# Kernel optimization log

Hardware: AMD Instinct MI355X
Metric: run time of the kernel (lower is better)

The kernel has to match this reference:

```python
import jax, jax.numpy as jnp
import numpy as np

T, N, F = 8, 4096, 128
LPF, HPF, H, LP_HID, E = 128, 128, 256, 256, 131072
D = LPF + HPF


def setup_inputs() -> dict:
    key = jax.random.key(0)
    ks = jax.random.split(key, 16)
    s = lambda k, *shape: jax.random.normal(k, shape, dtype=jnp.float32) * 0.05
    feats = jax.random.normal(ks[0], (T, N, F), dtype=jnp.float32)
    # row-stochastic-ish propagation matrices
    p = jax.random.uniform(ks[1], (T, N, N), dtype=jnp.float32)
    p = p / jnp.sum(p, axis=-1, keepdims=True)
    eidx = jax.random.randint(ks[2], (2, E), 0, N, dtype=jnp.int64)
    return {
        "features": feats,
        "p_matrix": p,
        "predict_edge_index": eidx,
        "W_lpf": s(ks[3], F, LPF), "b_lpf": jnp.zeros((LPF,), jnp.float32),
        "W_hpf": s(ks[4], F, HPF), "b_hpf": jnp.zeros((HPF,), jnp.float32),
        "W_ih": s(ks[5], 4 * H, D), "W_hh": s(ks[6], 4 * H, H),
        "b_ih": jnp.zeros((4 * H,), jnp.float32), "b_hh": jnp.zeros((4 * H,), jnp.float32),
        "W1": s(ks[7], 2 * H, LP_HID), "b1": jnp.zeros((LP_HID,), jnp.float32),
        "W2": s(ks[8], LP_HID, 1), "b2": jnp.zeros((1,), jnp.float32),
    }


def reference(features, p_matrix, predict_edge_index, W_lpf, b_lpf, W_hpf, b_hpf,
              W_ih, W_hh, b_ih, b_hh, W1, b1, W2, b2):
    # --- batched low/high-pass graph filters over all T snapshots ---
    xw = jnp.einsum('tnf,fd->tnd', features, W_lpf)          # X @ W_lp
    low = jax.nn.relu(jnp.einsum('tnm,tmd->tnd', p_matrix, xw) + b_lpf)
    px = jnp.einsum('tnm,tmf->tnf', p_matrix, features)      # P @ X
    high = jax.nn.relu(jnp.einsum('tnf,fd->tnd', features - px, W_hpf) + b_hpf)
    x_seq = jnp.concatenate([low, high], axis=-1)            # [T, N, D]

    # --- LSTM over time, nodes as batch (torch gate order i,f,g,o) ---
    def step(carry, x_t):
        h, c = carry
        gates = x_t @ W_ih.T + h @ W_hh.T + (b_ih + b_hh)    # [N, 4H]
        i, f, g, o = jnp.split(gates, 4, axis=-1)
        c = jax.nn.sigmoid(f) * c + jax.nn.sigmoid(i) * jnp.tanh(g)
        h = jax.nn.sigmoid(o) * jnp.tanh(c)
        return (h, c), None

    h0 = jnp.zeros((N, H), x_seq.dtype)
    (h_fin, _), _ = jax.lax.scan(step, (h0, h0), x_seq)      # final timestep hidden

    # --- gather + concat + MLP link predictor ---
    src = h_fin[predict_edge_index[0]]
    dst = h_fin[predict_edge_index[1]]
    comb = jnp.concatenate([src, dst], axis=-1)              # [E, 2H]
    hid = jax.nn.relu(comb @ W1 + b1)
    logits = (hid @ W2 + b2).squeeze(-1)                     # [E]
    return logits
```

## Files before the change

kernel.cpp:

```cpp
#include <hip/hip_runtime.h>
#include <stdint.h>

#define T_ 8
#define N_ 4096
#define E_ 131072

typedef __attribute__((ext_vector_type(4))) float f32x4;
typedef __attribute__((ext_vector_type(8))) short s16x8;
typedef __attribute__((ext_vector_type(4))) short s16x4;

static __device__ __forceinline__ short f2bf(float f) {
    union { float f; unsigned u; } v; v.f = f;
    unsigned r = v.u + 0x7fffu + ((v.u >> 16) & 1u);
    return (short)(r >> 16);
}
static __device__ __forceinline__ float bf2f(short s) {
    union { float f; unsigned u; } v; v.u = ((unsigned)(unsigned short)s) << 16;
    return v.f;
}

static __device__ __forceinline__ void bar_nodrain() {
    asm volatile("s_waitcnt lgkmcnt(0)\n\ts_barrier" ::: "memory");
}

__global__ __launch_bounds__(256) void xw_gemm(const float* __restrict__ A,
                                               const float* __restrict__ W,
                                               float* __restrict__ C) {
    __shared__ float As[32][68];
    __shared__ float Ws[32][132];
    const int m0 = blockIdx.x * 64;
    const int tid = threadIdx.x;
    const int rg = tid & 15, cg = tid >> 4;
    float acc[4][8];
#pragma unroll
    for (int r = 0; r < 4; r++)
#pragma unroll
        for (int c = 0; c < 8; c++) acc[r][c] = 0.f;

    for (int k0 = 0; k0 < 128; k0 += 32) {
#pragma unroll
        for (int s = 0; s < 2; s++) {
            int q = tid + s * 256, row = q >> 3, k4 = q & 7;
            f32x4 v = *(const f32x4*)&A[(size_t)(m0 + row) * 128 + k0 + k4 * 4];
#pragma unroll
            for (int i = 0; i < 4; i++) As[k4 * 4 + i][row] = v[i];
        }
#pragma unroll
        for (int s = 0; s < 4; s++) {
            int q = tid + s * 256, kk = q >> 5, j4 = q & 31;
            *(f32x4*)&Ws[kk][j4 * 4] = *(const f32x4*)&W[(size_t)(k0 + kk) * 128 + j4 * 4];
        }
        __syncthreads();
#pragma unroll
        for (int kk = 0; kk < 32; kk++) {
            f32x4 a  = *(const f32x4*)&As[kk][rg * 4];
            f32x4 w0 = *(const f32x4*)&Ws[kk][cg * 8];
            f32x4 w1 = *(const f32x4*)&Ws[kk][cg * 8 + 4];
#pragma unroll
            for (int r = 0; r < 4; r++)
#pragma unroll
                for (int c = 0; c < 4; c++) {
                    acc[r][c]     += a[r] * w0[c];
                    acc[r][c + 4] += a[r] * w1[c];
                }
        }
        __syncthreads();
    }
#pragma unroll
    for (int r = 0; r < 4; r++) {
        f32x4 o0 = {acc[r][0], acc[r][1], acc[r][2], acc[r][3]};
        f32x4 o1 = {acc[r][4], acc[r][5], acc[r][6], acc[r][7]};
        size_t base = (size_t)(m0 + rg * 4 + r) * 128 + cg * 8;
        *(f32x4*)&C[base] = o0;
        *(f32x4*)&C[base + 4] = o1;
    }
}

__global__ __launch_bounds__(256) void pack_yt(const float* __restrict__ xw,
                                               const float* __restrict__ feat,
                                               short* __restrict__ yt) {
    __shared__ float tile[32][33];
    const int t = blockIdx.z, j0 = blockIdx.y * 32, n0 = blockIdx.x * 32;
    const float* src = (j0 < 128) ? (xw + (size_t)t * N_ * 128 + j0)
                                  : (feat + (size_t)t * N_ * 128 + (j0 - 128));
    const int jj = threadIdx.x & 31, i4 = threadIdx.x >> 5;
#pragma unroll
    for (int s = 0; s < 4; s++) {
        int ii = i4 * 4 + s;
        tile[ii][jj] = src[(size_t)(n0 + ii) * 128 + jj];
    }
    __syncthreads();
    const int nn = threadIdx.x & 31, j4 = threadIdx.x >> 5;
#pragma unroll
    for (int s = 0; s < 4; s++) {
        int j2 = j4 * 4 + s;
        yt[(size_t)(t * 256 + j0 + j2) * N_ + n0 + nn] = f2bf(tile[nn][j2]);
    }
}

__global__ __launch_bounds__(512) void pfy_gemm(const float* __restrict__ P,
                                                const short* __restrict__ Yt,
                                                float* __restrict__ Z) {
    __shared__ short As[2][128][72];
    __shared__ short Bs[2][256][72];
    const int t = blockIdx.y;
    const int m0 = blockIdx.x * 128;
    const int tid = threadIdx.x;
    const int lane = tid & 63, wid = tid >> 6;
    const int wm = wid >> 2, wn = wid & 3;
    const int frow = lane & 15, kq = lane >> 4;

    const float* Pt = P + (size_t)t * N_ * N_;
    const short* Bt = Yt + (size_t)t * 256 * N_;

    const int ar = tid >> 2;
    const int ak16 = (tid & 3) * 16;
    const int bj = tid >> 1;
    const int bk32 = (tid & 1) * 32;

    f32x4 acc[4][4];
    f32x4 zf = {0.f, 0.f, 0.f, 0.f};
#pragma unroll
    for (int m = 0; m < 4; m++)
#pragma unroll
        for (int n = 0; n < 4; n++) acc[m][n] = zf;

    f32x4 aA[4], aB[4]; s16x8 bA[4], bB[4];

    const float* Pr = &Pt[(size_t)(m0 + ar) * 4096 + ak16];
    const short* Br = &Bt[(size_t)bj * 4096 + bk32];

#define LOADA(KT) do { const int k0_ = (KT) * 64;                              \
        _Pragma("unroll") for (int i = 0; i < 4; i++)                          \
            aA[i] = *(const f32x4*)&Pr[k0_ + i * 4];                           \
        _Pragma("unroll") for (int i = 0; i < 4; i++)                          \
            bA[i] = *(const s16x8*)&Br[k0_ + i * 8]; } while (0)
#define LOADB(KT) do { const int k0_ = (KT) * 64;                              \
        _Pragma("unroll") for (int i = 0; i < 4; i++)                          \
            aB[i] = *(const f32x4*)&Pr[k0_ + i * 4];                           \
        _Pragma("unroll") for (int i = 0; i < 4; i++)                          \
            bB[i] = *(const s16x8*)&Br[k0_ + i * 8]; } while (0)
#define STOREA(BUF) do {                                                       \
        _Pragma("unroll") for (int i = 0; i < 4; i++) {                        \
            s16x4 c4_;                                                         \
            _Pragma("unroll") for (int j = 0; j < 4; j++) c4_[j] = f2bf(aA[i][j]); \
            *(s16x4*)&As[BUF][ar][ak16 + i * 4] = c4_; }                       \
        _Pragma("unroll") for (int i = 0; i < 4; i++)                          \
            *(s16x8*)&Bs[BUF][bj][bk32 + i * 8] = bA[i]; } while (0)
#define STOREB(BUF) do {                                                       \
        _Pragma("unroll") for (int i = 0; i < 4; i++) {                        \
            s16x4 c4_;                                                         \
            _Pragma("unroll") for (int j = 0; j < 4; j++) c4_[j] = f2bf(aB[i][j]); \
            *(s16x4*)&As[BUF][ar][ak16 + i * 4] = c4_; }                       \
        _Pragma("unroll") for (int i = 0; i < 4; i++)                          \
            *(s16x8*)&Bs[BUF][bj][bk32 + i * 8] = bB[i]; } while (0)

    auto compute_t = [&](int buf) {
#pragma unroll
        for (int ks = 0; ks < 2; ks++) {
            s16x8 af[4], bfr[4];
#pragma unroll
            for (int m = 0; m < 4; m++)
                af[m] = *(const s16x8*)&As[buf][wm * 64 + m * 16 + frow][kq * 8 + ks * 32];
#pragma unroll
            for (int n = 0; n < 4; n++)
                bfr[n] = *(const s16x8*)&Bs[buf][wn * 64 + n * 16 + frow][kq * 8 + ks * 32];
#pragma unroll
            for (int m = 0; m < 4; m++)
#pragma unroll
                for (int n = 0; n < 4; n++)
                    acc[m][n] = __builtin_amdgcn_mfma_f32_16x16x32_bf16(af[m], bfr[n], acc[m][n], 0, 0, 0);
        }
    };

    LOADA(0);
    STOREA(0);
    LOADB(1);
    LOADA(2);
    bar_nodrain();

#pragma unroll 2
    for (int kt = 0; kt < 64; kt++) {
        compute_t(kt & 1);
        if (kt < 63) {
            if ((kt & 1) == 0) {
                STOREB(1);
                if (kt + 3 < 64) LOADB(kt + 3);
            } else {
                STOREA(0);
                if (kt + 3 < 64) LOADA(kt + 3);
            }
            bar_nodrain();
        }
    }
#undef LOADA
#undef LOADB
#undef STOREA
#undef STOREB

    float* Zt = Z + (size_t)t * N_ * 256;
#pragma unroll
    for (int m = 0; m < 4; m++)
#pragma unroll
        for (int n = 0; n < 4; n++)
#pragma unroll
            for (int r = 0; r < 4; r++) {
                int row = m0 + wm * 64 + m * 16 + kq * 4 + r;
                int col = wn * 64 + n * 16 + frow;
                Zt[(size_t)row * 256 + col] = acc[m][n][r];
            }
}

__global__ __launch_bounds__(256) void hp_gemm(const float* __restrict__ feat,
                                               const float* __restrict__ Z,
                                               const float* __restrict__ W,
                                               const float* __restrict__ b_hpf,
                                               const float* __restrict__ b_lpf,
                                               short* __restrict__ xhi,
                                               short* __restrict__ xlo) {
    __shared__ float As[32][68];
    __shared__ float Ws[32][132];
    const int m0 = blockIdx.x * 64;
    const int tid = threadIdx.x;
    const int rg = tid & 15, cg = tid >> 4;
    float acc[4][8];
#pragma unroll
    for (int r = 0; r < 4; r++)
#pragma unroll
        for (int c = 0; c < 8; c++) acc[r][c] = 0.f;

    for (int k0 = 0; k0 < 128; k0 += 32) {
#pragma unroll
        for (int s = 0; s < 2; s++) {
            int q = tid + s * 256, row = q >> 3, k4 = q & 7;
            f32x4 fv = *(const f32x4*)&feat[(size_t)(m0 + row) * 128 + k0 + k4 * 4];
            f32x4 zv = *(const f32x4*)&Z[(size_t)(m0 + row) * 256 + 128 + k0 + k4 * 4];
#pragma unroll
            for (int i = 0; i < 4; i++) As[k4 * 4 + i][row] = fv[i] - zv[i];
        }
#pragma unroll
        for (int s = 0; s < 4; s++) {
            int q = tid + s * 256, kk = q >> 5, j4 = q & 31;
            *(f32x4*)&Ws[kk][j4 * 4] = *(const f32x4*)&W[(size_t)(k0 + kk) * 128 + j4 * 4];
        }
        __syncthreads();
#pragma unroll
        for (int kk = 0; kk < 32; kk++) {
            f32x4 a  = *(const f32x4*)&As[kk][rg * 4];
            f32x4 w0 = *(const f32x4*)&Ws[kk][cg * 8];
            f32x4 w1 = *(const f32x4*)&Ws[kk][cg * 8 + 4];
#pragma unroll
            for (int r = 0; r < 4; r++)
#pragma unroll
                for (int c = 0; c < 4; c++) {
                    acc[r][c]     += a[r] * w0[c];
                    acc[r][c + 4] += a[r] * w1[c];
                }
        }
        __syncthreads();
    }
    float bh[8];
#pragma unroll
    for (int c = 0; c < 8; c++) bh[c] = b_hpf[cg * 8 + c];
#pragma unroll
    for (int r = 0; r < 4; r++) {
        s16x4 h0, h1, l0, l1;
#pragma unroll
        for (int c = 0; c < 4; c++) {
            float v0 = fmaxf(acc[r][c] + bh[c], 0.f);
            float v1 = fmaxf(acc[r][c + 4] + bh[c + 4], 0.f);
            h0[c] = f2bf(v0); l0[c] = f2bf(v0 - bf2f(h0[c]));
            h1[c] = f2bf(v1); l1[c] = f2bf(v1 - bf2f(h1[c]));
        }
        size_t base = (size_t)(m0 + rg * 4 + r) * 256 + 128 + cg * 8;
        *(s16x4*)&xhi[base] = h0;  *(s16x4*)&xhi[base + 4] = h1;
        *(s16x4*)&xlo[base] = l0;  *(s16x4*)&xlo[base + 4] = l1;
    }
#pragma unroll
    for (int s = 0; s < 8; s++) {
        int q = tid + s * 256, row = q >> 5, j4 = q & 31;
        f32x4 z = *(const f32x4*)&Z[(size_t)(m0 + row) * 256 + j4 * 4];
        f32x4 bb = *(const f32x4*)&b_lpf[j4 * 4];
        s16x4 hi, lo;
#pragma unroll
        for (int i = 0; i < 4; i++) {
            float v = fmaxf(z[i] + bb[i], 0.f);
            hi[i] = f2bf(v); lo[i] = f2bf(v - bf2f(hi[i]));
        }
        size_t base = (size_t)(m0 + row) * 256 + j4 * 4;
        *(s16x4*)&xhi[base] = hi;
        *(s16x4*)&xlo[base] = lo;
    }
}

__global__ __launch_bounds__(256) void pack_wc(const float* __restrict__ W_ih,
                                               const float* __restrict__ W_hh,
                                               short* __restrict__ whi,
                                               short* __restrict__ wlo) {
    int idx = (blockIdx.x * 256 + threadIdx.x) * 4;
    int j = idx >> 9, k = idx & 511;
    int orig = (j & 3) * 256 + (j >> 2);
    const float* src = (k < 256) ? &W_ih[(size_t)orig * 256 + k]
                                 : &W_hh[(size_t)orig * 256 + (k - 256)];
    f32x4 v = *(const f32x4*)src;
    s16x4 hi, lo;
#pragma unroll
    for (int i = 0; i < 4; i++) {
        hi[i] = f2bf(v[i]);
        lo[i] = f2bf(v[i] - bf2f(hi[i]));
    }
    *(s16x4*)&whi[idx] = hi;
    *(s16x4*)&wlo[idx] = lo;
}

__global__ void pack_bias(const float* __restrict__ b_ih,
                          const float* __restrict__ b_hh,
                          float* __restrict__ bsum) {
    int j = blockIdx.x * 256 + threadIdx.x;
    int orig = (j & 3) * 256 + (j >> 2);
    bsum[j] = b_ih[orig] + b_hh[orig];
}

__global__ __launch_bounds__(512) void lstm_step(const short* __restrict__ xhi,
                                                 const short* __restrict__ xlo,
                                                 const short* __restrict__ hhi_r,
                                                 const short* __restrict__ hlo_r,
                                                 const short* __restrict__ wchi,
                                                 const short* __restrict__ wclo,
                                                 const float* __restrict__ bsum,
                                                 float* __restrict__ cbuf,
                                                 short* __restrict__ hhi_w,
                                                 short* __restrict__ hlo_w) {
    __shared__ short Ah[2][128][40], Al[2][128][40];
    __shared__ short Bh[2][128][40], Bl[2][128][40];
    __shared__ float gl[128][132];
    const int m0 = blockIdx.x * 128;
    const int j0 = blockIdx.y * 128;
    const int tid = threadIdx.x;
    const int lane = tid & 63, wid = tid >> 6;
    const int wm = wid >> 2, wn = wid & 3;
    const int frow = lane & 15, kq = lane >> 4;

    const int sr = tid >> 2;
    const int sk8 = (tid & 3) * 8;

    f32x4 acc[4][2];
    f32x4 zf = {0.f, 0.f, 0.f, 0.f};
#pragma unroll
    for (int m = 0; m < 4; m++)
#pragma unroll
        for (int n = 0; n < 2; n++) acc[m][n] = zf;

    s16x8 a_h, a_l, b_h, b_l;

    auto load_t = [&](int kt) {
        const int k0 = kt * 32;
        const short* ah = (k0 < 256) ? xhi : hhi_r;
        const short* al = (k0 < 256) ? xlo : hlo_r;
        const size_t abase = (size_t)(m0 + sr) * 256 + (k0 & 255) + sk8;
        a_h = *(const s16x8*)&ah[abase];
        a_l = *(const s16x8*)&al[abase];
        const size_t bb = (size_t)(j0 + sr) * 512 + k0 + sk8;
        b_h = *(const s16x8*)&wchi[bb];
        b_l = *(const s16x8*)&wclo[bb];
    };
    auto store_t = [&](int buf) {
        *(s16x8*)&Ah[buf][sr][sk8] = a_h;
        *(s16x8*)&Al[buf][sr][sk8] = a_l;
        *(s16x8*)&Bh[buf][sr][sk8] = b_h;
        *(s16x8*)&Bl[buf][sr][sk8] = b_l;
    };
    auto compute_t = [&](int buf) {
        s16x8 afh[4], afl[4], bfh[2], bfl[2];
#pragma unroll
        for (int m = 0; m < 4; m++) {
            afh[m] = *(const s16x8*)&Ah[buf][wm * 64 + m * 16 + frow][kq * 8];
            afl[m] = *(const s16x8*)&Al[buf][wm * 64 + m * 16 + frow][kq * 8];
        }
#pragma unroll
        for (int n = 0; n < 2; n++) {
            bfh[n] = *(const s16x8*)&Bh[buf][wn * 32 + n * 16 + frow][kq * 8];
            bfl[n] = *(const s16x8*)&Bl[buf][wn * 32 + n * 16 + frow][kq * 8];
        }
#pragma unroll
        for (int m = 0; m < 4; m++)
#pragma unroll
            for (int n = 0; n < 2; n++) {
                acc[m][n] = __builtin_amdgcn_mfma_f32_16x16x32_bf16(afh[m], bfh[n], acc[m][n], 0, 0, 0);
                acc[m][n] = __builtin_amdgcn_mfma_f32_16x16x32_bf16(afh[m], bfl[n], acc[m][n], 0, 0, 0);
                acc[m][n] = __builtin_amdgcn_mfma_f32_16x16x32_bf16(afl[m], bfh[n], acc[m][n], 0, 0, 0);
            }
    };

    load_t(0);
    store_t(0);
    bar_nodrain();
#pragma unroll 2
    for (int kt = 0; kt < 16; kt++) {
        const int cur = kt & 1;
        if (kt < 15) load_t(kt + 1);
        compute_t(cur);
        bar_nodrain();
        if (kt < 15) { store_t(cur ^ 1); bar_nodrain(); }
    }

#pragma unroll
    for (int m = 0; m < 4; m++)
#pragma unroll
        for (int n = 0; n < 2; n++)
#pragma unroll
            for (int r = 0; r < 4; r++)
                gl[wm * 64 + m * 16 + kq * 4 + r][wn * 32 + n * 16 + frow] = acc[m][n][r];
    bar_nodrain();

    const int erow = tid >> 2;
    const int ec0 = (tid & 3) * 8;
    const size_t cbase = (size_t)(m0 + erow) * 256 + blockIdx.y * 32 + ec0;
    f32x4 co0 = *(const f32x4*)&cbuf[cbase];
    f32x4 co1 = *(const f32x4*)&cbuf[cbase + 4];
    f32x4 cn0, cn1;
    s16x8 h8, l8;
#pragma unroll
    for (int i = 0; i < 8; i++) {
        f32x4 g4 = *(const f32x4*)&gl[erow][(ec0 + i) * 4];
        f32x4 bs = *(const f32x4*)&bsum[j0 + (ec0 + i) * 4];
        float si = 1.f / (1.f + expf(-(g4[0] + bs[0])));
        float sf = 1.f / (1.f + expf(-(g4[1] + bs[1])));
        float tg = tanhf(g4[2] + bs[2]);
        float so = 1.f / (1.f + expf(-(g4[3] + bs[3])));
        float cold = (i < 4) ? co0[i] : co1[i - 4];
        float cn = sf * cold + si * tg;
        float hv = so * tanhf(cn);
        if (i < 4) cn0[i] = cn; else cn1[i - 4] = cn;
        h8[i] = f2bf(hv);
        l8[i] = f2bf(hv - bf2f(h8[i]));
    }
    *(f32x4*)&cbuf[cbase] = cn0;
    *(f32x4*)&cbuf[cbase + 4] = cn1;
    *(s16x8*)&hhi_w[cbase] = h8;
    *(s16x8*)&hlo_w[cbase] = l8;
}

__global__ __launch_bounds__(256) void pack_w1c(const float* __restrict__ W1,
                                                short* __restrict__ whi,
                                                short* __restrict__ wlo) {
    __shared__ float tile[32][33];
    const int k0 = blockIdx.x * 32;
    const int j0 = blockIdx.y * 32;
    const int koff = (j0 >= 256) ? 256 : 0;
    const int joff = (j0 >= 256) ? 256 : 0;
    const int jj = threadIdx.x & 31, k4 = threadIdx.x >> 5;
#pragma unroll
    for (int s = 0; s < 4; s++) {
        int kk = k4 * 4 + s;
        tile[kk][jj] = W1[(size_t)(k0 + kk + koff) * 256 + (j0 + jj - joff)];
    }
    __syncthreads();
    const int kk2 = threadIdx.x & 31, j4 = threadIdx.x >> 5;
#pragma unroll
    for (int s = 0; s < 4; s++) {
        int j2 = j4 * 4 + s;
        float v = tile[kk2][j2];
        short hb = f2bf(v);
        whi[(size_t)(j0 + j2) * 256 + k0 + kk2] = hb;
        wlo[(size_t)(j0 + j2) * 256 + k0 + kk2] = f2bf(v - bf2f(hb));
    }
}

__global__ __launch_bounds__(512) void uv_gemm(const short* __restrict__ hhi,
                                               const short* __restrict__ hlo,
                                               const short* __restrict__ whi,
                                               const short* __restrict__ wlo,
                                               float* __restrict__ UV) {
    __shared__ short Ah[2][128][40], Al[2][128][40];
    __shared__ short Bh[2][128][40], Bl[2][128][40];
    const int m0 = blockIdx.x * 128;
    const int j0 = blockIdx.y * 128;
    const int tid = threadIdx.x;
    const int lane = tid & 63, wid = tid >> 6;
    const int wm = wid >> 2, wn = wid & 3;
    const int frow = lane & 15, kq = lane >> 4;
    const int sr = tid >> 2;
    const int sk8 = (tid & 3) * 8;

    f32x4 acc[4][2];
    f32x4 zf = {0.f, 0.f, 0.f, 0.f};
#pragma unroll
    for (int m = 0; m < 4; m++)
#pragma unroll
        for (int n = 0; n < 2; n++) acc[m][n] = zf;

    s16x8 a_h, a_l, b_h, b_l;

    auto load_t = [&](int kt) {
        const int k0 = kt * 32;
        const size_t abase = (size_t)(m0 + sr) * 256 + k0 + sk8;
        a_h = *(const s16x8*)&hhi[abase];
        a_l = *(const s16x8*)&hlo[abase];
        const size_t bb = (size_t)(j0 + sr) * 256 + k0 + sk8;
        b_h = *(const s16x8*)&whi[bb];
        b_l = *(const s16x8*)&wlo[bb];
    };
    auto store_t = [&](int buf) {
        *(s16x8*)&Ah[buf][sr][sk8] = a_h;
        *(s16x8*)&Al[buf][sr][sk8] = a_l;
        *(s16x8*)&Bh[buf][sr][sk8] = b_h;
        *(s16x8*)&Bl[buf][sr][sk8] = b_l;
    };
    auto compute_t = [&](int buf) {
        s16x8 afh[4], afl[4], bfh[2], bfl[2];
#pragma unroll
        for (int m = 0; m < 4; m++) {
            afh[m] = *(const s16x8*)&Ah[buf][wm * 64 + m * 16 + frow][kq * 8];
            afl[m] = *(const s16x8*)&Al[buf][wm * 64 + m * 16 + frow][kq * 8];
        }
#pragma unroll
        for (int n = 0; n < 2; n++) {
            bfh[n] = *(const s16x8*)&Bh[buf][wn * 32 + n * 16 + frow][kq * 8];
            bfl[n] = *(const s16x8*)&Bl[buf][wn * 32 + n * 16 + frow][kq * 8];
        }
#pragma unroll
        for (int m = 0; m < 4; m++)
#pragma unroll
            for (int n = 0; n < 2; n++) {
                acc[m][n] = __builtin_amdgcn_mfma_f32_16x16x32_bf16(afh[m], bfh[n], acc[m][n], 0, 0, 0);
                acc[m][n] = __builtin_amdgcn_mfma_f32_16x16x32_bf16(afh[m], bfl[n], acc[m][n], 0, 0, 0);
                acc[m][n] = __builtin_amdgcn_mfma_f32_16x16x32_bf16(afl[m], bfh[n], acc[m][n], 0, 0, 0);
            }
    };

    load_t(0);
    store_t(0);
    bar_nodrain();
#pragma unroll 2
    for (int kt = 0; kt < 8; kt++) {
        const int cur = kt & 1;
        if (kt < 7) load_t(kt + 1);
        compute_t(cur);
        bar_nodrain();
        if (kt < 7) { store_t(cur ^ 1); bar_nodrain(); }
    }

#pragma unroll
    for (int m = 0; m < 4; m++)
#pragma unroll
        for (int n = 0; n < 2; n++)
#pragma unroll
            for (int r = 0; r < 4; r++) {
                int row = m0 + wm * 64 + m * 16 + kq * 4 + r;
                int col = j0 + wn * 32 + n * 16 + frow;
                UV[(size_t)row * 512 + col] = acc[m][n][r];
            }
}

__global__ __launch_bounds__(256) void mlp_edge(const float* __restrict__ UV,
                                                const int* __restrict__ eidx,
                                                const float* __restrict__ b1,
                                                const float* __restrict__ W2,
                                                const float* __restrict__ b2,
                                                float* __restrict__ out) {
    const int e = blockIdx.x * 4 + (threadIdx.x >> 6);
    const int lane = threadIdx.x & 63;
    const int c4 = lane * 4;
    const int src = eidx[e];
    const int dst = eidx[E_ + e];
    f32x4 u = *(const f32x4*)&UV[(size_t)src * 512 + c4];
    f32x4 v = *(const f32x4*)&UV[(size_t)dst * 512 + 256 + c4];
    f32x4 bb = *(const f32x4*)&b1[c4];
    f32x4 ww = *(const f32x4*)&W2[c4];
    float p = 0.f;
#pragma unroll
    for (int i = 0; i < 4; i++)
        p += fmaxf(u[i] + v[i] + bb[i], 0.f) * ww[i];
    p += __shfl_xor(p, 1);
    p += __shfl_xor(p, 2);
    p += __shfl_xor(p, 4);
    p += __shfl_xor(p, 8);
    p += __shfl_xor(p, 16);
    p += __shfl_xor(p, 32);
    if (lane == 0) out[e] = p + b2[0];
}

extern "C" void kernel_launch(void* const* d_in, const int* in_sizes, int n_in,
                              void* d_out, int out_size, void* d_ws, size_t ws_size,
                              hipStream_t stream) {
    (void)in_sizes; (void)n_in; (void)out_size; (void)ws_size;
    const float* feat  = (const float*)d_in[0];
    const float* P     = (const float*)d_in[1];
    const int*   eidx  = (const int*)d_in[2];
    const float* W_lpf = (const float*)d_in[3];
    const float* b_lpf = (const float*)d_in[4];
    const float* W_hpf = (const float*)d_in[5];
    const float* b_hpf = (const float*)d_in[6];
    const float* W_ih  = (const float*)d_in[7];
    const float* W_hh  = (const float*)d_in[8];
    const float* b_ih  = (const float*)d_in[9];
    const float* b_hh  = (const float*)d_in[10];
    const float* W1    = (const float*)d_in[11];
    const float* b1    = (const float*)d_in[12];
    const float* W2    = (const float*)d_in[13];
    const float* b2    = (const float*)d_in[14];
    float* out = (float*)d_out;

    char* ws = (char*)d_ws;
    float* xw    = (float*)ws;   ws += (size_t)T_ * N_ * 128 * 4;
    char*  ytreg = ws;           ws += (size_t)T_ * 256 * N_ * 2;
    char*  Zreg  = ws;           ws += (size_t)T_ * N_ * 256 * 4;
    short* xhi   = (short*)ws;   ws += (size_t)T_ * N_ * 256 * 2;
    short* xlo   = (short*)ws;   ws += (size_t)T_ * N_ * 256 * 2;

    short* yt    = (short*)ytreg;
    float* Z     = (float*)Zreg;
    float* cbuf  = (float*)ytreg;
    short* hhi0  = (short*)(ytreg + (size_t)N_ * 256 * 4);
    short* hlo0  = hhi0 + (size_t)N_ * 256;
    short* hhi1  = hlo0 + (size_t)N_ * 256;
    short* hlo1  = hhi1 + (size_t)N_ * 256;
    short* w1chi = (short*)Zreg;
    short* w1clo = w1chi + (size_t)512 * 256;
    short* wchi  = w1clo + (size_t)512 * 256;
    short* wclo  = wchi + (size_t)1024 * 512;
    float* bsum  = (float*)(wclo + (size_t)1024 * 512);
    float* UV    = bsum + 1024;

    xw_gemm<<<dim3(T_ * N_ / 64), 256, 0, stream>>>(feat, W_lpf, xw);
    pack_yt<<<dim3(N_ / 32, 8, T_), 256, 0, stream>>>(xw, feat, yt);
    pfy_gemm<<<dim3(N_ / 128, T_), 512, 0, stream>>>(P, yt, Z);
    hp_gemm<<<dim3(T_ * N_ / 64), 256, 0, stream>>>(feat, Z, W_hpf, b_hpf, b_lpf, xhi, xlo);

    pack_w1c<<<dim3(8, 16), 256, 0, stream>>>(W1, w1chi, w1clo);
    pack_wc<<<dim3(1024 * 512 / 1024), 256, 0, stream>>>(W_ih, W_hh, wchi, wclo);
    pack_bias<<<dim3(4), 256, 0, stream>>>(b_ih, b_hh, bsum);

    hipMemsetAsync(ytreg, 0, (size_t)N_ * 256 * 4 + (size_t)N_ * 256 * 2 * 2, stream);

    for (int t = 0; t < T_; t++) {
        const short* hr_hi = (t & 1) ? hhi1 : hhi0;
        const short* hr_lo = (t & 1) ? hlo1 : hlo0;
        short* hw_hi = (t & 1) ? hhi0 : hhi1;
        short* hw_lo = (t & 1) ? hlo0 : hlo1;
        lstm_step<<<dim3(N_ / 128, 1024 / 128), 512, 0, stream>>>(
            xhi + (size_t)t * N_ * 256, xlo + (size_t)t * N_ * 256,
            hr_hi, hr_lo, wchi, wclo, bsum, cbuf, hw_hi, hw_lo);
    }

    uv_gemm<<<dim3(N_ / 128, 512 / 128), 512, 0, stream>>>(hhi0, hlo0, w1chi, w1clo, UV);
    mlp_edge<<<dim3(E_ / 4), 256, 0, stream>>>(UV, eidx, b1, W2, b2, out);
}
```

Baseline: 435.9 us.

## Reassociate low-pass filter as (P@X)@W_lp to halve big GEMM width

Uses associativity so P@(X@W_lp) becomes (P@X)@W_lp. The large P GEMM now only multiplies by X (128 columns instead of 256), and both filters are applied afterwards by one small GEMM kernel with a mode grid dimension. This removes the xw_gemm kernel and halves the MFMA work and B-operand traffic in pfy_gemm, while the P reads stay the same. The trade is a second small GEMM over P@X and a different bf16 rounding path for the low-pass branch.

```diff
diff --git a/kernel.cpp b/kernel.cpp
--- a/kernel.cpp
+++ b/kernel.cpp
@@ -23,66 +23,11 @@
     asm volatile("s_waitcnt lgkmcnt(0)\n\ts_barrier" ::: "memory");
 }
 
-__global__ __launch_bounds__(256) void xw_gemm(const float* __restrict__ A,
-                                               const float* __restrict__ W,
-                                               float* __restrict__ C) {
-    __shared__ float As[32][68];
-    __shared__ float Ws[32][132];
-    const int m0 = blockIdx.x * 64;
-    const int tid = threadIdx.x;
-    const int rg = tid & 15, cg = tid >> 4;
-    float acc[4][8];
-#pragma unroll
-    for (int r = 0; r < 4; r++)
-#pragma unroll
-        for (int c = 0; c < 8; c++) acc[r][c] = 0.f;
-
-    for (int k0 = 0; k0 < 128; k0 += 32) {
-#pragma unroll
-        for (int s = 0; s < 2; s++) {
-            int q = tid + s * 256, row = q >> 3, k4 = q & 7;
-            f32x4 v = *(const f32x4*)&A[(size_t)(m0 + row) * 128 + k0 + k4 * 4];
-#pragma unroll
-            for (int i = 0; i < 4; i++) As[k4 * 4 + i][row] = v[i];
-        }
-#pragma unroll
-        for (int s = 0; s < 4; s++) {
-            int q = tid + s * 256, kk = q >> 5, j4 = q & 31;
-            *(f32x4*)&Ws[kk][j4 * 4] = *(const f32x4*)&W[(size_t)(k0 + kk) * 128 + j4 * 4];
-        }
-        __syncthreads();
-#pragma unroll
-        for (int kk = 0; kk < 32; kk++) {
-            f32x4 a  = *(const f32x4*)&As[kk][rg * 4];
-            f32x4 w0 = *(const f32x4*)&Ws[kk][cg * 8];
-            f32x4 w1 = *(const f32x4*)&Ws[kk][cg * 8 + 4];
-#pragma unroll
-            for (int r = 0; r < 4; r++)
-#pragma unroll
-                for (int c = 0; c < 4; c++) {
-                    acc[r][c]     += a[r] * w0[c];
-                    acc[r][c + 4] += a[r] * w1[c];
-                }
-        }
-        __syncthreads();
-    }
-#pragma unroll
-    for (int r = 0; r < 4; r++) {
-        f32x4 o0 = {acc[r][0], acc[r][1], acc[r][2], acc[r][3]};
-        f32x4 o1 = {acc[r][4], acc[r][5], acc[r][6], acc[r][7]};
-        size_t base = (size_t)(m0 + rg * 4 + r) * 128 + cg * 8;
-        *(f32x4*)&C[base] = o0;
-        *(f32x4*)&C[base + 4] = o1;
-    }
-}
-
-__global__ __launch_bounds__(256) void pack_yt(const float* __restrict__ xw,
-                                               const float* __restrict__ feat,
+__global__ __launch_bounds__(256) void pack_yt(const float* __restrict__ feat,
                                                short* __restrict__ yt) {
     __shared__ float tile[32][33];
     const int t = blockIdx.z, j0 = blockIdx.y * 32, n0 = blockIdx.x * 32;
-    const float* src = (j0 < 128) ? (xw + (size_t)t * N_ * 128 + j0)
-                                  : (feat + (size_t)t * N_ * 128 + (j0 - 128));
+    const float* src = feat + (size_t)t * N_ * 128 + j0;
     const int jj = threadIdx.x & 31, i4 = threadIdx.x >> 5;
 #pragma unroll
     for (int s = 0; s < 4; s++) {
@@ -94,7 +39,7 @@
 #pragma unroll
     for (int s = 0; s < 4; s++) {
         int j2 = j4 * 4 + s;
-        yt[(size_t)(t * 256 + j0 + j2) * N_ + n0 + nn] = f2bf(tile[nn][j2]);
+        yt[(size_t)(t * 128 + j0 + j2) * N_ + n0 + nn] = f2bf(tile[nn][j2]);
     }
 }
 
@@ -102,7 +47,7 @@
                                                 const short* __restrict__ Yt,
                                                 float* __restrict__ Z) {
     __shared__ short As[2][128][72];
-    __shared__ short Bs[2][256][72];
+    __shared__ short Bs[2][128][72];
     const int t = blockIdx.y;
     const int m0 = blockIdx.x * 128;
     const int tid = threadIdx.x;
@@ -111,64 +56,64 @@
     const int frow = lane & 15, kq = lane >> 4;
 
     const float* Pt = P + (size_t)t * N_ * N_;
-    const short* Bt = Yt + (size_t)t * 256 * N_;
+    const short* Bt = Yt + (size_t)t * 128 * N_;
 
     const int ar = tid >> 2;
     const int ak16 = (tid & 3) * 16;
-    const int bj = tid >> 1;
-    const int bk32 = (tid & 1) * 32;
-
-    f32x4 acc[4][4];
+    const int bj = tid >> 2;
+    const int bk16 = (tid & 3) * 16;
+
+    f32x4 acc[4][2];
     f32x4 zf = {0.f, 0.f, 0.f, 0.f};
 #pragma unroll
     for (int m = 0; m < 4; m++)
 #pragma unroll
-        for (int n = 0; n < 4; n++) acc[m][n] = zf;
-
-    f32x4 aA[4], aB[4]; s16x8 bA[4], bB[4];
+        for (int n = 0; n < 2; n++) acc[m][n] = zf;
+
+    f32x4 aA[4], aB[4]; s16x8 bA[2], bB[2];
 
     const float* Pr = &Pt[(size_t)(m0 + ar) * 4096 + ak16];
-    const short* Br = &Bt[(size_t)bj * 4096 + bk32];
+    const short* Br = &Bt[(size_t)bj * 4096 + bk16];
 
 #define LOADA(KT) do { const int k0_ = (KT) * 64;                              \
         _Pragma("unroll") for (int i = 0; i < 4; i++)                          \
             aA[i] = *(const f32x4*)&Pr[k0_ + i * 4];                           \
-        _Pragma("unroll") for (int i = 0; i < 4; i++)                          \
+        _Pragma("unroll") for (int i = 0; i < 2; i++)                          \
             bA[i] = *(const s16x8*)&Br[k0_ + i * 8]; } while (0)
 #define LOADB(KT) do { const int k0_ = (KT) * 64;                              \
         _Pragma("unroll") for (int i = 0; i < 4; i++)                          \
             aB[i] = *(const f32x4*)&Pr[k0_ + i * 4];                           \
-        _Pragma("unroll") for (int i = 0; i < 4; i++)                          \
+        _Pragma("unroll") for (int i = 0; i < 2; i++)                          \
             bB[i] = *(const s16x8*)&Br[k0_ + i * 8]; } while (0)
 #define STOREA(BUF) do {                                                       \
         _Pragma("unroll") for (int i = 0; i < 4; i++) {                        \
             s16x4 c4_;                                                         \
             _Pragma("unroll") for (int j = 0; j < 4; j++) c4_[j] = f2bf(aA[i][j]); \
             *(s16x4*)&As[BUF][ar][ak16 + i * 4] = c4_; }                       \
-        _Pragma("unroll") for (int i = 0; i < 4; i++)                          \
-            *(s16x8*)&Bs[BUF][bj][bk32 + i * 8] = bA[i]; } while (0)
+        _Pragma("unroll") for (int i = 0; i < 2; i++)                          \
+            *(s16x8*)&Bs[BUF][bj][bk16 + i * 8] = bA[i]; } while (0)
 #define STOREB(BUF) do {                                                       \
         _Pragma("unroll") for (int i = 0; i < 4; i++) {                        \
             s16x4 c4_;                                                         \
             _Pragma("unroll") for (int j = 0; j < 4; j++) c4_[j] = f2bf(aB[i][j]); \
             *(s16x4*)&As[BUF][ar][ak16 + i * 4] = c4_; }                       \
-        _Pragma("unroll") for (int i = 0; i < 4; i++)                          \
-            *(s16x8*)&Bs[BUF][bj][bk32 + i * 8] = bB[i]; } while (0)
+        _Pragma("unroll") for (int i = 0; i < 2; i++)                          \
+            *(s16x8*)&Bs[BUF][bj][bk16 + i * 8] = bB[i]; } while (0)
 
     auto compute_t = [&](int buf) {
 #pragma unroll
         for (int ks = 0; ks < 2; ks++) {
-            s16x8 af[4], bfr[4];
+            s16x8 af[4], bfr[2];
 #pragma unroll
             for (int m = 0; m < 4; m++)
                 af[m] = *(const s16x8*)&As[buf][wm * 64 + m * 16 + frow][kq * 8 + ks * 32];
 #pragma unroll
-            for (int n = 0; n < 4; n++)
-                bfr[n] = *(const s16x8*)&Bs[buf][wn * 64 + n * 16 + frow][kq * 8 + ks * 32];
+            for (int n = 0; n < 2; n++)
+                bfr[n] = *(const s16x8*)&Bs[buf][wn * 32 + n * 16 + frow][kq * 8 + ks * 32];
 #pragma unroll
             for (int m = 0; m < 4; m++)
 #pragma unroll
-                for (int n = 0; n < 4; n++)
+                for (int n = 0; n < 2; n++)
                     acc[m][n] = __builtin_amdgcn_mfma_f32_16x16x32_bf16(af[m], bfr[n], acc[m][n], 0, 0, 0);
         }
     };
@@ -198,29 +143,33 @@
 #undef STOREA
 #undef STOREB
 
-    float* Zt = Z + (size_t)t * N_ * 256;
+    float* Zt = Z + (size_t)t * N_ * 128;
 #pragma unroll
     for (int m = 0; m < 4; m++)
 #pragma unroll
-        for (int n = 0; n < 4; n++)
+        for (int n = 0; n < 2; n++)
 #pragma unroll
             for (int r = 0; r < 4; r++) {
                 int row = m0 + wm * 64 + m * 16 + kq * 4 + r;
-                int col = wn * 64 + n * 16 + frow;
-                Zt[(size_t)row * 256 + col] = acc[m][n][r];
+                int col = wn * 32 + n * 16 + frow;
+                Zt[(size_t)row * 128 + col] = acc[m][n][r];
             }
 }
 
-__global__ __launch_bounds__(256) void hp_gemm(const float* __restrict__ feat,
-                                               const float* __restrict__ Z,
-                                               const float* __restrict__ W,
-                                               const float* __restrict__ b_hpf,
-                                               const float* __restrict__ b_lpf,
-                                               short* __restrict__ xhi,
-                                               short* __restrict__ xlo) {
+__global__ __launch_bounds__(256) void hp2_gemm(const float* __restrict__ feat,
+                                                const float* __restrict__ PX,
+                                                const float* __restrict__ Wlp,
+                                                const float* __restrict__ Whp,
+                                                const float* __restrict__ b_lpf,
+                                                const float* __restrict__ b_hpf,
+                                                short* __restrict__ xhi,
+                                                short* __restrict__ xlo) {
     __shared__ float As[32][68];
     __shared__ float Ws[32][132];
     const int m0 = blockIdx.x * 64;
+    const int mode = blockIdx.y;
+    const float* W = mode ? Whp : Wlp;
+    const float* bp = mode ? b_hpf : b_lpf;
     const int tid = threadIdx.x;
     const int rg = tid & 15, cg = tid >> 4;
     float acc[4][8];
@@ -233,10 +182,17 @@
 #pragma unroll
         for (int s = 0; s < 2; s++) {
             int q = tid + s * 256, row = q >> 3, k4 = q & 7;
-            f32x4 fv = *(const f32x4*)&feat[(size_t)(m0 + row) * 128 + k0 + k4 * 4];
-            f32x4 zv = *(const f32x4*)&Z[(size_t)(m0 + row) * 256 + 128 + k0 + k4 * 4];
-#pragma unroll
-            for (int i = 0; i < 4; i++) As[k4 * 4 + i][row] = fv[i] - zv[i];
+            f32x4 pv = *(const f32x4*)&PX[(size_t)(m0 + row) * 128 + k0 + k4 * 4];
+            f32x4 v;
+            if (mode) {
+                f32x4 fv = *(const f32x4*)&feat[(size_t)(m0 + row) * 128 + k0 + k4 * 4];
+#pragma unroll
+                for (int i = 0; i < 4; i++) v[i] = fv[i] - pv[i];
+            } else {
+                v = pv;
+            }
+#pragma unroll
+            for (int i = 0; i < 4; i++) As[k4 * 4 + i][row] = v[i];
         }
 #pragma unroll
         for (int s = 0; s < 4; s++) {
@@ -261,7 +217,7 @@
     }
     float bh[8];
 #pragma unroll
-    for (int c = 0; c < 8; c++) bh[c] = b_hpf[cg * 8 + c];
+    for (int c = 0; c < 8; c++) bh[c] = bp[cg * 8 + c];
 #pragma unroll
     for (int r = 0; r < 4; r++) {
         s16x4 h0, h1, l0, l1;
@@ -272,24 +228,9 @@
             h0[c] = f2bf(v0); l0[c] = f2bf(v0 - bf2f(h0[c]));
             h1[c] = f2bf(v1); l1[c] = f2bf(v1 - bf2f(h1[c]));
         }
-        size_t base = (size_t)(m0 + rg * 4 + r) * 256 + 128 + cg * 8;
+        size_t base = (size_t)(m0 + rg * 4 + r) * 256 + mode * 128 + cg * 8;
         *(s16x4*)&xhi[base] = h0;  *(s16x4*)&xhi[base + 4] = h1;
         *(s16x4*)&xlo[base] = l0;  *(s16x4*)&xlo[base + 4] = l1;
-    }
-#pragma unroll
-    for (int s = 0; s < 8; s++) {
-        int q = tid + s * 256, row = q >> 5, j4 = q & 31;
-        f32x4 z = *(const f32x4*)&Z[(size_t)(m0 + row) * 256 + j4 * 4];
-        f32x4 bb = *(const f32x4*)&b_lpf[j4 * 4];
-        s16x4 hi, lo;
-#pragma unroll
-        for (int i = 0; i < 4; i++) {
-            float v = fmaxf(z[i] + bb[i], 0.f);
-            hi[i] = f2bf(v); lo[i] = f2bf(v - bf2f(hi[i]));
-        }
-        size_t base = (size_t)(m0 + row) * 256 + j4 * 4;
-        *(s16x4*)&xhi[base] = hi;
-        *(s16x4*)&xlo[base] = lo;
     }
 }
 
@@ -608,9 +549,10 @@
     char*  Zreg  = ws;           ws += (size_t)T_ * N_ * 256 * 4;
     short* xhi   = (short*)ws;   ws += (size_t)T_ * N_ * 256 * 2;
     short* xlo   = (short*)ws;   ws += (size_t)T_ * N_ * 256 * 2;
+    (void)xw;
 
     short* yt    = (short*)ytreg;
-    float* Z     = (float*)Zreg;
+    float* PX    = (float*)Zreg;
     float* cbuf  = (float*)ytreg;
     short* hhi0  = (short*)(ytreg + (size_t)N_ * 256 * 4);
     short* hlo0  = hhi0 + (size_t)N_ * 256;
@@ -623,10 +565,10 @@
     float* bsum  = (float*)(wclo + (size_t)1024 * 512);
     float* UV    = bsum + 1024;
 
-    xw_gemm<<<dim3(T_ * N_ / 64), 256, 0, stream>>>(feat, W_lpf, xw);
-    pack_yt<<<dim3(N_ / 32, 8, T_), 256, 0, stream>>>(xw, feat, yt);
-    pfy_gemm<<<dim3(N_ / 128, T_), 512, 0, stream>>>(P, yt, Z);
-    hp_gemm<<<dim3(T_ * N_ / 64), 256, 0, stream>>>(feat, Z, W_hpf, b_hpf, b_lpf, xhi, xlo);
+    pack_yt<<<dim3(N_ / 32, 4, T_), 256, 0, stream>>>(feat, yt);
+    pfy_gemm<<<dim3(N_ / 128, T_), 512, 0, stream>>>(P, yt, PX);
+    hp2_gemm<<<dim3(T_ * N_ / 64, 2), 256, 0, stream>>>(feat, PX, W_lpf, W_hpf,
+                                                        b_lpf, b_hpf, xhi, xlo);
 
     pack_w1c<<<dim3(8, 16), 256, 0, stream>>>(W1, w1chi, w1clo);
     pack_wc<<<dim3(1024 * 512 / 1024), 256, 0, stream>>>(W_ih, W_hh, wchi, wclo);
```

New measurement: 407.5 us. 6.5% less time.
